# Kernel optimization log

Hardware: AMD Instinct MI355X
Metric: run time of the kernel (lower is better)

Reference implementation:

```python
import jax, jax.numpy as jnp
import numpy as np

N = 50000   # n_nodes
E = 800000  # n_edges (directed)
D = 64      # feature dim (in = hidden = out = 64 per source)


def setup_inputs() -> dict:
    key = jax.random.key(0)
    ks = jax.random.split(key, 16)
    s = 0.1  # init scale
    inp = {
        "x": jax.random.normal(ks[0], (N, D), jnp.float32),
        "edge_index": jax.random.randint(ks[1], (2, E), 0, N),
        # GCNConv 1
        "W1": jax.random.normal(ks[2], (D, 64), jnp.float32) * s,
        "b1": jnp.zeros((64,), jnp.float32),
        # TransformerConv (heads=1): query/key/value + root (skip) linear
        "Wq": jax.random.normal(ks[3], (64, 64), jnp.float32) * s,
        "bq": jnp.zeros((64,), jnp.float32),
        "Wk": jax.random.normal(ks[4], (64, 64), jnp.float32) * s,
        "bk": jnp.zeros((64,), jnp.float32),
        "Wv": jax.random.normal(ks[5], (64, 64), jnp.float32) * s,
        "bv": jnp.zeros((64,), jnp.float32),
        "Ws": jax.random.normal(ks[6], (64, 64), jnp.float32) * s,
        "bs": jnp.zeros((64,), jnp.float32),
        # GCNConv 2
        "W2": jax.random.normal(ks[7], (64, D), jnp.float32) * s,
        "b2": jnp.zeros((D,), jnp.float32),
    }
    return inp


def gcn_conv(x, W, b, src, dst, n):
    """PyG GCNConv: symmetric normalization with self-loops, then scatter-add."""
    xw = x @ W  # [N, F]
    loop = jnp.arange(n)
    src2 = jnp.concatenate([src, loop])
    dst2 = jnp.concatenate([dst, loop])
    deg = jax.ops.segment_sum(jnp.ones(src2.shape[0], xw.dtype), dst2, num_segments=n)
    dinv = jnp.where(deg > 0, jax.lax.rsqrt(deg), 0.0)
    norm = dinv[src2] * dinv[dst2]  # [E+N]
    out = jax.ops.segment_sum(xw[src2] * norm[:, None], dst2, num_segments=n)
    return out + b


def segment_softmax(logits, seg, n):
    m = jax.ops.segment_max(logits, seg, num_segments=n)
    e = jnp.exp(logits - m[seg])
    z = jax.ops.segment_sum(e, seg, num_segments=n)
    return e / z[seg]


def transformer_conv(x, Wq, bq, Wk, bk, Wv, bv, Ws, bs, src, dst, n):
    """PyG TransformerConv (heads=1, concat=True, root_weight=True)."""
    q = x @ Wq + bq  # [N, 64]
    k = x @ Wk + bk
    v = x @ Wv + bv
    scale = jax.lax.rsqrt(jnp.asarray(q.shape[-1], q.dtype))
    logits = jnp.sum(q[dst] * k[src], axis=-1) * scale  # [E]
    alpha = segment_softmax(logits, dst, n)
    aggr = jax.ops.segment_sum(v[src] * alpha[:, None], dst, num_segments=n)
    return aggr + x @ Ws + bs  # root/skip connection


def reference(x, edge_index, W1, b1, Wq, bq, Wk, bk, Wv, bv, Ws, bs, W2, b2):
    src, dst = edge_index[0], edge_index[1]
    n = x.shape[0]
    x1 = jax.nn.relu(gcn_conv(x, W1, b1, src, dst, n))
    x2 = transformer_conv(x1, Wq, bq, Wk, bk, Wv, bv, Ws, bs, src, dst, n)
    x3 = gcn_conv(x2, W2, b2, src, dst, n)
    return x3
```

## Files before the change

### kernel.cpp

```cpp
#include <hip/hip_runtime.h>
#include <math.h>


#define D 64
#define BKT_SHIFT 9
#define CAP 12288
#define CHUNK 4096

__device__ __forceinline__ unsigned short f2bf(float f) {
    unsigned int u = __float_as_uint(f);
    u += 0x7FFFu + ((u >> 16) & 1u);
    return (unsigned short)(u >> 16);
}
#define BF_LO(u) __uint_as_float((u) << 16)
#define BF_HI(u) __uint_as_float((u) & 0xFFFF0000u)


__global__ void init_gcursor(int* __restrict__ gcursor) {
    if (threadIdx.x < 128) gcursor[threadIdx.x] = 0;
}

__global__ __launch_bounds__(256) void binA_kernel(const int* __restrict__ src,
                                                   const int* __restrict__ dst,
                                                   int* __restrict__ gcursor,
                                                   unsigned int* __restrict__ staging,
                                                   int e, int nbkt) {
    __shared__ int cntB[128];
    __shared__ int offB[128];
    __shared__ int curB[128];
    __shared__ int gbase[128];
    __shared__ unsigned int pairs[CHUNK];
    __shared__ unsigned char bkt[CHUNK];

    int t = threadIdx.x;
    int e0 = blockIdx.x * CHUNK;
    int ecnt = min(CHUNK, e - e0);

    if (t < 128) cntB[t] = 0;
    __syncthreads();

    int myS[CHUNK / 256], myD[CHUNK / 256];
    #pragma unroll
    for (int i = 0; i < CHUNK / 256; ++i) {
        int idx = t + 256 * i;
        if (idx < ecnt) {
            myS[i] = src[e0 + idx];
            myD[i] = dst[e0 + idx];
            atomicAdd(&cntB[myD[i] >> BKT_SHIFT], 1);
        }
    }
    __syncthreads();
    if (t < 128) offB[t] = cntB[t];
    __syncthreads();
    for (int off = 1; off < 128; off <<= 1) {
        int add = (t < 128 && t >= off) ? offB[t - off] : 0;
        __syncthreads();
        if (t < 128) offB[t] += add;
        __syncthreads();
    }
    if (t < 128) {
        int excl = offB[t] - cntB[t];
        offB[t] = excl;
        curB[t] = excl;
        if (t < nbkt && cntB[t] > 0) gbase[t] = atomicAdd(&gcursor[t], cntB[t]);
    }
    __syncthreads();
    #pragma unroll
    for (int i = 0; i < CHUNK / 256; ++i) {
        int idx = t + 256 * i;
        if (idx < ecnt) {
            int b = myD[i] >> BKT_SHIFT;
            int p = atomicAdd(&curB[b], 1);
            pairs[p] = ((unsigned int)myD[i] << 16) | (unsigned int)myS[i];
            bkt[p] = (unsigned char)b;
        }
    }
    __syncthreads();
    for (int p = t; p < ecnt; p += 256) {
        int b = bkt[p];
        staging[(size_t)b * CAP + gbase[b] + (p - offB[b])] = pairs[p];
    }
}

__global__ __launch_bounds__(256) void binB_kernel(const int* __restrict__ gcursor,
                                                   const unsigned int* __restrict__ staging,
                                                   unsigned short* __restrict__ esrc,
                                                   int* __restrict__ cnt,
                                                   int* __restrict__ rowptr,
                                                   float* __restrict__ dinv,
                                                   int n, int nbkt) {
    __shared__ int bpre[128];
    __shared__ int c512[512];
    __shared__ int o512[512];
    int t = threadIdx.x;
    int b = blockIdx.x;

    if (t < 128) bpre[t] = (t < nbkt) ? gcursor[t] : 0;
    __syncthreads();
    for (int off = 1; off < 128; off <<= 1) {
        int add = (t < 128 && t >= off) ? bpre[t - off] : 0;
        __syncthreads();
        if (t < 128) bpre[t] += add;
        __syncthreads();
    }
    int base_b = (b == 0) ? 0 : bpre[b - 1];
    int cnt_b = gcursor[b];
    int lo = b << BKT_SHIFT;

    c512[t] = 0; c512[t + 256] = 0;
    __syncthreads();
    const unsigned int* st = staging + (size_t)b * CAP;
    for (int i = t; i < cnt_b; i += 256)
        atomicAdd(&c512[(int)(st[i] >> 16) - lo], 1);
    __syncthreads();
    o512[t] = c512[t]; o512[t + 256] = c512[t + 256];
    __syncthreads();
    for (int off = 1; off < 512; off <<= 1) {
        int a1 = (t >= off) ? o512[t - off] : 0;
        int a2 = o512[t + 256 - off];
        __syncthreads();
        o512[t] += a1; o512[t + 256] += a2;
        __syncthreads();
    }
    int e1 = o512[t] - c512[t];
    int e2 = o512[t + 256] - c512[t + 256];
    __syncthreads();
    o512[t] = e1; o512[t + 256] = e2;
    __syncthreads();
    for (int i = t; i < 512; i += 256) {
        int g = lo + i;
        if (g < n) {
            int c = c512[i];
            cnt[g] = c;
            rowptr[g] = base_b + o512[i];
            dinv[g] = rsqrtf((float)c + 1.0f);
        }
    }
    __syncthreads();
    for (int i = t; i < cnt_b; i += 256) {
        unsigned int pk = st[i];
        int local = (int)(pk >> 16) - lo;
        int p = atomicAdd(&o512[local], 1);
        esrc[base_b + p] = (unsigned short)(pk & 0xFFFFu);
    }
}

__global__ __launch_bounds__(256) void gemm64_bf16s(const float* __restrict__ X,
                                                    const float* __restrict__ W,
                                                    const float* __restrict__ dinv,
                                                    unsigned short* __restrict__ xs, int n) {
    __shared__ float sX[64][68];
    __shared__ float sW[64 * 64];
    int t = threadIdx.x;
    int base = blockIdx.x * 64;
    #pragma unroll
    for (int i = 0; i < 4; ++i) {
        int f = t * 4 + i * 1024;
        *(float4*)&sW[f] = *(const float4*)&W[f];
        int r = f >> 6, c = f & 63;
        int row = base + r;
        float4 xv = (row < n) ? *(const float4*)&X[(size_t)row * D + c]
                              : make_float4(0.f, 0.f, 0.f, 0.f);
        *(float4*)&sX[r][c] = xv;
    }
    __syncthreads();

    int cg = t & 15, rg = t >> 4;
    int j0 = cg * 4, r0 = rg * 4;
    float acc[4][4];
    #pragma unroll
    for (int a = 0; a < 4; ++a)
        #pragma unroll
        for (int c = 0; c < 4; ++c) acc[a][c] = 0.0f;

    #pragma unroll 4
    for (int kk = 0; kk < 64; kk += 4) {
        float4 w0 = *(const float4*)&sW[(kk + 0) * 64 + j0];
        float4 w1 = *(const float4*)&sW[(kk + 1) * 64 + j0];
        float4 w2 = *(const float4*)&sW[(kk + 2) * 64 + j0];
        float4 w3 = *(const float4*)&sW[(kk + 3) * 64 + j0];
        #pragma unroll
        for (int a = 0; a < 4; ++a) {
            float4 xv = *(const float4*)&sX[r0 + a][kk];
            acc[a][0] = fmaf(xv.x, w0.x, acc[a][0]); acc[a][1] = fmaf(xv.x, w0.y, acc[a][1]);
            acc[a][2] = fmaf(xv.x, w0.z, acc[a][2]); acc[a][3] = fmaf(xv.x, w0.w, acc[a][3]);
            acc[a][0] = fmaf(xv.y, w1.x, acc[a][0]); acc[a][1] = fmaf(xv.y, w1.y, acc[a][1]);
            acc[a][2] = fmaf(xv.y, w1.z, acc[a][2]); acc[a][3] = fmaf(xv.y, w1.w, acc[a][3]);
            acc[a][0] = fmaf(xv.z, w2.x, acc[a][0]); acc[a][1] = fmaf(xv.z, w2.y, acc[a][1]);
            acc[a][2] = fmaf(xv.z, w2.z, acc[a][2]); acc[a][3] = fmaf(xv.z, w2.w, acc[a][3]);
            acc[a][0] = fmaf(xv.w, w3.x, acc[a][0]); acc[a][1] = fmaf(xv.w, w3.y, acc[a][1]);
            acc[a][2] = fmaf(xv.w, w3.z, acc[a][2]); acc[a][3] = fmaf(xv.w, w3.w, acc[a][3]);
        }
    }

    #pragma unroll
    for (int a = 0; a < 4; ++a) {
        int row = base + r0 + a;
        if (row < n) {
            float dv = dinv[row];
            ushort4 h;
            h.x = f2bf(acc[a][0] * dv);
            h.y = f2bf(acc[a][1] * dv);
            h.z = f2bf(acc[a][2] * dv);
            h.w = f2bf(acc[a][3] * dv);
            *(ushort4*)&xs[(size_t)row * D + j0] = h;
        }
    }
}

__global__ __launch_bounds__(256) void fusedA_kernel(const unsigned short* __restrict__ xs,
                                                     const float* __restrict__ dinv,
                                                     const int* __restrict__ rowptr,
                                                     const int* __restrict__ cnt,
                                                     const unsigned short* __restrict__ esrc,
                                                     const float* __restrict__ b1,
                                                     const float* __restrict__ Wq,
                                                     const float* __restrict__ bq,
                                                     const float* __restrict__ Wk,
                                                     const float* __restrict__ bk,
                                                     const float* __restrict__ Wv,
                                                     const float* __restrict__ bv,
                                                     const float* __restrict__ Ws,
                                                     const float* __restrict__ bs,
                                                     float* __restrict__ Yq,
                                                     unsigned short* __restrict__ kv,
                                                     float* __restrict__ Ysk, int n) {
    __shared__ float sX[32][68];
    __shared__ float sW[64 * 64];
    int t = threadIdx.x;
    int base = blockIdx.x * 32;
    int local = t >> 3, sub = t & 7;
    int j0 = sub * 8;
    int node = base + local;

    {
        float a[8] = {0.f, 0.f, 0.f, 0.f, 0.f, 0.f, 0.f, 0.f};
        float4 o0 = make_float4(0.f, 0.f, 0.f, 0.f);
        float4 o1 = make_float4(0.f, 0.f, 0.f, 0.f);
        if (node < n) {
            float dd = dinv[node];
            int start = rowptr[node], deg = cnt[node];
            uint4 sr = *(const uint4*)&xs[(size_t)node * D + j0];
            a[0] += BF_LO(sr.x); a[1] += BF_HI(sr.x);
            a[2] += BF_LO(sr.y); a[3] += BF_HI(sr.y);
            a[4] += BF_LO(sr.z); a[5] += BF_HI(sr.z);
            a[6] += BF_LO(sr.w); a[7] += BF_HI(sr.w);
            int i = 0;
            for (; i + 8 <= deg; i += 8) {
                uint4 r[8];
                #pragma unroll
                for (int u = 0; u < 8; ++u) {
                    int s = esrc[start + i + u];
                    r[u] = *(const uint4*)&xs[(size_t)s * D + j0];
                }
                #pragma unroll
                for (int u = 0; u < 8; ++u) {
                    a[0] += BF_LO(r[u].x); a[1] += BF_HI(r[u].x);
                    a[2] += BF_LO(r[u].y); a[3] += BF_HI(r[u].y);
                    a[4] += BF_LO(r[u].z); a[5] += BF_HI(r[u].z);
                    a[6] += BF_LO(r[u].w); a[7] += BF_HI(r[u].w);
                }
            }
            for (; i + 4 <= deg; i += 4) {
                uint4 r[4];
                #pragma unroll
                for (int u = 0; u < 4; ++u) {
                    int s = esrc[start + i + u];
                    r[u] = *(const uint4*)&xs[(size_t)s * D + j0];
                }
                #pragma unroll
                for (int u = 0; u < 4; ++u) {
                    a[0] += BF_LO(r[u].x); a[1] += BF_HI(r[u].x);
                    a[2] += BF_LO(r[u].y); a[3] += BF_HI(r[u].y);
                    a[4] += BF_LO(r[u].z); a[5] += BF_HI(r[u].z);
                    a[6] += BF_LO(r[u].w); a[7] += BF_HI(r[u].w);
                }
            }
            for (; i < deg; ++i) {
                int s = esrc[start + i];
                uint4 r = *(const uint4*)&xs[(size_t)s * D + j0];
                a[0] += BF_LO(r.x); a[1] += BF_HI(r.x);
                a[2] += BF_LO(r.y); a[3] += BF_HI(r.y);
                a[4] += BF_LO(r.z); a[5] += BF_HI(r.z);
                a[6] += BF_LO(r.w); a[7] += BF_HI(r.w);
            }
            float4 bb0 = *(const float4*)&b1[j0];
            float4 bb1 = *(const float4*)&b1[j0 + 4];
            o0.x = fmaxf(fmaf(dd, a[0], bb0.x), 0.f);
            o0.y = fmaxf(fmaf(dd, a[1], bb0.y), 0.f);
            o0.z = fmaxf(fmaf(dd, a[2], bb0.z), 0.f);
            o0.w = fmaxf(fmaf(dd, a[3], bb0.w), 0.f);
            o1.x = fmaxf(fmaf(dd, a[4], bb1.x), 0.f);
            o1.y = fmaxf(fmaf(dd, a[5], bb1.y), 0.f);
            o1.z = fmaxf(fmaf(dd, a[6], bb1.z), 0.f);
            o1.w = fmaxf(fmaf(dd, a[7], bb1.w), 0.f);
        }
        *(float4*)&sX[local][j0] = o0;
        *(float4*)&sX[local][j0 + 4] = o1;
    }

    int cg = t & 15, rg = t >> 4;
    int gj0 = cg * 4, r0 = rg * 2;

    #pragma unroll 1
    for (int w4 = 0; w4 < 4; ++w4) {
        const float* W = (w4 == 0) ? Wq : (w4 == 1) ? Wk : (w4 == 2) ? Wv : Ws;
        const float* B = (w4 == 0) ? bq : (w4 == 1) ? bk : (w4 == 2) ? bv : bs;
        __syncthreads();
        #pragma unroll
        for (int i = 0; i < 4; ++i) {
            int f = t * 4 + i * 1024;
            *(float4*)&sW[f] = *(const float4*)&W[f];
        }
        __syncthreads();

        float acc[2][4];
        #pragma unroll
        for (int a = 0; a < 2; ++a)
            #pragma unroll
            for (int c = 0; c < 4; ++c) acc[a][c] = 0.0f;

        #pragma unroll 4
        for (int kk = 0; kk < 64; kk += 4) {
            float4 w0 = *(const float4*)&sW[(kk + 0) * 64 + gj0];
            float4 w1 = *(const float4*)&sW[(kk + 1) * 64 + gj0];
            float4 w2 = *(const float4*)&sW[(kk + 2) * 64 + gj0];
            float4 w3 = *(const float4*)&sW[(kk + 3) * 64 + gj0];
            #pragma unroll
            for (int a = 0; a < 2; ++a) {
                float4 xv = *(const float4*)&sX[r0 + a][kk];
                acc[a][0] = fmaf(xv.x, w0.x, acc[a][0]); acc[a][1] = fmaf(xv.x, w0.y, acc[a][1]);
                acc[a][2] = fmaf(xv.x, w0.z, acc[a][2]); acc[a][3] = fmaf(xv.x, w0.w, acc[a][3]);
                acc[a][0] = fmaf(xv.y, w1.x, acc[a][0]); acc[a][1] = fmaf(xv.y, w1.y, acc[a][1]);
                acc[a][2] = fmaf(xv.y, w1.z, acc[a][2]); acc[a][3] = fmaf(xv.y, w1.w, acc[a][3]);
                acc[a][0] = fmaf(xv.z, w2.x, acc[a][0]); acc[a][1] = fmaf(xv.z, w2.y, acc[a][1]);
                acc[a][2] = fmaf(xv.z, w2.z, acc[a][2]); acc[a][3] = fmaf(xv.z, w2.w, acc[a][3]);
                acc[a][0] = fmaf(xv.w, w3.x, acc[a][0]); acc[a][1] = fmaf(xv.w, w3.y, acc[a][1]);
                acc[a][2] = fmaf(xv.w, w3.z, acc[a][2]); acc[a][3] = fmaf(xv.w, w3.w, acc[a][3]);
            }
        }

        float4 bb = *(const float4*)&B[gj0];
        if (w4 == 0) {
            #pragma unroll
            for (int a = 0; a < 2; ++a) {
                int row = base + r0 + a;
                if (row < n) {
                    float4 o = make_float4((acc[a][0] + bb.x) * 0.125f,
                                           (acc[a][1] + bb.y) * 0.125f,
                                           (acc[a][2] + bb.z) * 0.125f,
                                           (acc[a][3] + bb.w) * 0.125f);
                    *(float4*)&Yq[(size_t)row * D + gj0] = o;
                }
            }
        } else if (w4 == 3) {
            #pragma unroll
            for (int a = 0; a < 2; ++a) {
                int row = base + r0 + a;
                if (row < n) {
                    float4 o = make_float4(acc[a][0] + bb.x, acc[a][1] + bb.y,
                                           acc[a][2] + bb.z, acc[a][3] + bb.w);
                    *(float4*)&Ysk[(size_t)row * D + gj0] = o;
                }
            }
        } else {
            int off = (w4 == 1) ? 0 : 64;
            #pragma unroll
            for (int a = 0; a < 2; ++a) {
                int row = base + r0 + a;
                if (row < n) {
                    ushort4 h;
                    h.x = f2bf(acc[a][0] + bb.x);
                    h.y = f2bf(acc[a][1] + bb.y);
                    h.z = f2bf(acc[a][2] + bb.z);
                    h.w = f2bf(acc[a][3] + bb.w);
                    *(ushort4*)&kv[(size_t)row * 128 + off + gj0] = h;
                }
            }
        }
    }
}

__global__ __launch_bounds__(256) void fusedB_kernel(const float* __restrict__ q,
                                                     const unsigned short* __restrict__ kv,
                                                     const float* __restrict__ skip,
                                                     const float* __restrict__ dinv,
                                                     const int* __restrict__ rowptr,
                                                     const int* __restrict__ cnt,
                                                     const unsigned short* __restrict__ esrc,
                                                     const float* __restrict__ W2,
                                                     unsigned short* __restrict__ xs2, int n) {
    __shared__ float sX[32][68];
    __shared__ float sW[64 * 64];
    int t = threadIdx.x;
    int base = blockIdx.x * 32;
    int local = t >> 3, sub = t & 7;
    int j0 = sub * 8;
    int node = base + local;

    #pragma unroll
    for (int i = 0; i < 4; ++i) {
        int f = t * 4 + i * 1024;
        *(float4*)&sW[f] = *(const float4*)&W2[f];
    }

    {
        float4 o0 = make_float4(0.f, 0.f, 0.f, 0.f);
        float4 o1 = make_float4(0.f, 0.f, 0.f, 0.f);
        if (node < n) {
            int start = rowptr[node], deg = cnt[node];
            float4 q0 = *(const float4*)&q[(size_t)node * D + j0];
            float4 q1 = *(const float4*)&q[(size_t)node * D + j0 + 4];
            float4 s0 = *(const float4*)&skip[(size_t)node * D + j0];
            float4 s1 = *(const float4*)&skip[(size_t)node * D + j0 + 4];
            float z = 0.0f;
            float a[8] = {0.f, 0.f, 0.f, 0.f, 0.f, 0.f, 0.f, 0.f};
            int i = 0;
            for (; i + 8 <= deg; i += 8) {
                size_t ro[8];
                #pragma unroll
                for (int u = 0; u < 8; ++u)
                    ro[u] = (size_t)esrc[start + i + u] * 128;
                float w[8];
                {
                    uint4 kr[8];
                    #pragma unroll
                    for (int u = 0; u < 8; ++u)
                        kr[u] = *(const uint4*)&kv[ro[u] + j0];
                    float p[8];
                    #pragma unroll
                    for (int u = 0; u < 8; ++u)
                        p[u] = q0.x * BF_LO(kr[u].x) + q0.y * BF_HI(kr[u].x)
                             + q0.z * BF_LO(kr[u].y) + q0.w * BF_HI(kr[u].y)
                             + q1.x * BF_LO(kr[u].z) + q1.y * BF_HI(kr[u].z)
                             + q1.z * BF_LO(kr[u].w) + q1.w * BF_HI(kr[u].w);
                    #pragma unroll
                    for (int off = 1; off < 8; off <<= 1) {
                        #pragma unroll
                        for (int u = 0; u < 8; ++u) p[u] += __shfl_xor(p[u], off, 64);
                    }
                    #pragma unroll
                    for (int u = 0; u < 8; ++u) {
                        w[u] = __expf(p[u]);
                        z += w[u];
                    }
                }
                {
                    uint4 vr[8];
                    #pragma unroll
                    for (int u = 0; u < 8; ++u)
                        vr[u] = *(const uint4*)&kv[ro[u] + 64 + j0];
                    #pragma unroll
                    for (int u = 0; u < 8; ++u) {
                        a[0] = fmaf(w[u], BF_LO(vr[u].x), a[0]);
                        a[1] = fmaf(w[u], BF_HI(vr[u].x), a[1]);
                        a[2] = fmaf(w[u], BF_LO(vr[u].y), a[2]);
                        a[3] = fmaf(w[u], BF_HI(vr[u].y), a[3]);
                        a[4] = fmaf(w[u], BF_LO(vr[u].z), a[4]);
                        a[5] = fmaf(w[u], BF_HI(vr[u].z), a[5]);
                        a[6] = fmaf(w[u], BF_LO(vr[u].w), a[6]);
                        a[7] = fmaf(w[u], BF_HI(vr[u].w), a[7]);
                    }
                }
            }
            for (; i < deg; ++i) {
                size_t ro = (size_t)esrc[start + i] * 128;
                uint4 kr = *(const uint4*)&kv[ro + j0];
                uint4 vr = *(const uint4*)&kv[ro + 64 + j0];
                float p = q0.x * BF_LO(kr.x) + q0.y * BF_HI(kr.x)
                        + q0.z * BF_LO(kr.y) + q0.w * BF_HI(kr.y)
                        + q1.x * BF_LO(kr.z) + q1.y * BF_HI(kr.z)
                        + q1.z * BF_LO(kr.w) + q1.w * BF_HI(kr.w);
                #pragma unroll
                for (int off = 1; off < 8; off <<= 1) p += __shfl_xor(p, off, 64);
                float w = __expf(p);
                z += w;
                a[0] = fmaf(w, BF_LO(vr.x), a[0]); a[1] = fmaf(w, BF_HI(vr.x), a[1]);
                a[2] = fmaf(w, BF_LO(vr.y), a[2]); a[3] = fmaf(w, BF_HI(vr.y), a[3]);
                a[4] = fmaf(w, BF_LO(vr.z), a[4]); a[5] = fmaf(w, BF_HI(vr.z), a[5]);
                a[6] = fmaf(w, BF_LO(vr.w), a[6]); a[7] = fmaf(w, BF_HI(vr.w), a[7]);
            }
            if (deg > 0) {
                float inv = 1.0f / z;
                o0.x = fmaf(a[0], inv, s0.x); o0.y = fmaf(a[1], inv, s0.y);
                o0.z = fmaf(a[2], inv, s0.z); o0.w = fmaf(a[3], inv, s0.w);
                o1.x = fmaf(a[4], inv, s1.x); o1.y = fmaf(a[5], inv, s1.y);
                o1.z = fmaf(a[6], inv, s1.z); o1.w = fmaf(a[7], inv, s1.w);
            } else {
                o0 = s0; o1 = s1;
            }
        }
        *(float4*)&sX[local][j0] = o0;
        *(float4*)&sX[local][j0 + 4] = o1;
    }
    __syncthreads();

    int cg = t & 15, rg = t >> 4;
    int gj0 = cg * 4, r0 = rg * 2;
    float acc[2][4];
    #pragma unroll
    for (int a = 0; a < 2; ++a)
        #pragma unroll
        for (int c = 0; c < 4; ++c) acc[a][c] = 0.0f;

    #pragma unroll 4
    for (int kk = 0; kk < 64; kk += 4) {
        float4 w0 = *(const float4*)&sW[(kk + 0) * 64 + gj0];
        float4 w1 = *(const float4*)&sW[(kk + 1) * 64 + gj0];
        float4 w2 = *(const float4*)&sW[(kk + 2) * 64 + gj0];
        float4 w3 = *(const float4*)&sW[(kk + 3) * 64 + gj0];
        #pragma unroll
        for (int a = 0; a < 2; ++a) {
            float4 xv = *(const float4*)&sX[r0 + a][kk];
            acc[a][0] = fmaf(xv.x, w0.x, acc[a][0]); acc[a][1] = fmaf(xv.x, w0.y, acc[a][1]);
            acc[a][2] = fmaf(xv.x, w0.z, acc[a][2]); acc[a][3] = fmaf(xv.x, w0.w, acc[a][3]);
            acc[a][0] = fmaf(xv.y, w1.x, acc[a][0]); acc[a][1] = fmaf(xv.y, w1.y, acc[a][1]);
            acc[a][2] = fmaf(xv.y, w1.z, acc[a][2]); acc[a][3] = fmaf(xv.y, w1.w, acc[a][3]);
            acc[a][0] = fmaf(xv.z, w2.x, acc[a][0]); acc[a][1] = fmaf(xv.z, w2.y, acc[a][1]);
            acc[a][2] = fmaf(xv.z, w2.z, acc[a][2]); acc[a][3] = fmaf(xv.z, w2.w, acc[a][3]);
            acc[a][0] = fmaf(xv.w, w3.x, acc[a][0]); acc[a][1] = fmaf(xv.w, w3.y, acc[a][1]);
            acc[a][2] = fmaf(xv.w, w3.z, acc[a][2]); acc[a][3] = fmaf(xv.w, w3.w, acc[a][3]);
        }
    }

    #pragma unroll
    for (int a = 0; a < 2; ++a) {
        int row = base + r0 + a;
        if (row < n) {
            float dv = dinv[row];
            ushort4 h;
            h.x = f2bf(acc[a][0] * dv);
            h.y = f2bf(acc[a][1] * dv);
            h.z = f2bf(acc[a][2] * dv);
            h.w = f2bf(acc[a][3] * dv);
            *(ushort4*)&xs2[(size_t)row * D + gj0] = h;
        }
    }
}

__global__ __launch_bounds__(256) void gcn_gather_kernel(const unsigned short* __restrict__ xs,
                                                         const float* __restrict__ dinv,
                                                         const int* __restrict__ rowptr,
                                                         const int* __restrict__ cnt,
                                                         const unsigned short* __restrict__ esrc,
                                                         const float* __restrict__ bias,
                                                         float* __restrict__ out,
                                                         int n, int relu) {
    int node = (blockIdx.x * blockDim.x + threadIdx.x) >> 6;
    if (node >= n) return;
    int lane = threadIdx.x & 63;
    int grp = lane >> 3;
    int sub = lane & 7;
    int j0 = sub * 8;

    int start = rowptr[node], deg = cnt[node];

    float a[8] = {0.f, 0.f, 0.f, 0.f, 0.f, 0.f, 0.f, 0.f};
    int i = grp;
    int sNext = (i < deg) ? esrc[start + i] : 0;
    for (; i < deg; i += 8) {
        int s = sNext;
        int in = i + 8;
        if (in < deg) sNext = esrc[start + in];
        uint4 r = *(const uint4*)&xs[(size_t)s * D + j0];
        a[0] += BF_LO(r.x); a[1] += BF_HI(r.x);
        a[2] += BF_LO(r.y); a[3] += BF_HI(r.y);
        a[4] += BF_LO(r.z); a[5] += BF_HI(r.z);
        a[6] += BF_LO(r.w); a[7] += BF_HI(r.w);
    }
    #pragma unroll
    for (int off = 8; off < 64; off <<= 1) {
        #pragma unroll
        for (int c = 0; c < 8; ++c) a[c] += __shfl_xor(a[c], off, 64);
    }

    if (grp == 0) {
        float dd = dinv[node];
        uint4 sr = *(const uint4*)&xs[(size_t)node * D + j0];
        a[0] += BF_LO(sr.x); a[1] += BF_HI(sr.x);
        a[2] += BF_LO(sr.y); a[3] += BF_HI(sr.y);
        a[4] += BF_LO(sr.z); a[5] += BF_HI(sr.z);
        a[6] += BF_LO(sr.w); a[7] += BF_HI(sr.w);
        float4 b0 = *(const float4*)&bias[j0];
        float4 b1 = *(const float4*)&bias[j0 + 4];
        float o[8];
        o[0] = fmaf(dd, a[0], b0.x); o[1] = fmaf(dd, a[1], b0.y);
        o[2] = fmaf(dd, a[2], b0.z); o[3] = fmaf(dd, a[3], b0.w);
        o[4] = fmaf(dd, a[4], b1.x); o[5] = fmaf(dd, a[5], b1.y);
        o[6] = fmaf(dd, a[6], b1.z); o[7] = fmaf(dd, a[7], b1.w);
        if (relu) {
            #pragma unroll
            for (int c = 0; c < 8; ++c) o[c] = fmaxf(o[c], 0.f);
        }
        *(float4*)&out[(size_t)node * D + j0] = make_float4(o[0], o[1], o[2], o[3]);
        *(float4*)&out[(size_t)node * D + j0 + 4] = make_float4(o[4], o[5], o[6], o[7]);
    }
}


extern "C" void kernel_launch(void* const* d_in, const int* in_sizes, int n_in,
                              void* d_out, int out_size, void* d_ws, size_t ws_size,
                              hipStream_t stream) {
    const float* x  = (const float*)d_in[0];
    const int*   ei = (const int*)d_in[1];
    const float* W1 = (const float*)d_in[2];
    const float* b1 = (const float*)d_in[3];
    const float* Wq = (const float*)d_in[4];
    const float* bq = (const float*)d_in[5];
    const float* Wk = (const float*)d_in[6];
    const float* bk = (const float*)d_in[7];
    const float* Wv = (const float*)d_in[8];
    const float* bv = (const float*)d_in[9];
    const float* Ws = (const float*)d_in[10];
    const float* bs = (const float*)d_in[11];
    const float* W2 = (const float*)d_in[12];
    const float* b2 = (const float*)d_in[13];
    float* out = (float*)d_out;

    const int n = in_sizes[0] / D;
    const int e = in_sizes[1] / 2;
    const int* src = ei;
    const int* dst = ei + e;
    const int n64 = n * D;
    const int nbkt = (n + (1 << BKT_SHIFT) - 1) >> BKT_SHIFT;

    char* w = (char*)d_ws;
    auto carve = [&](size_t bytes) {
        char* p = w;
        w += (bytes + 255) & ~(size_t)255;
        return p;
    };
    int* gcursor            = (int*)carve(128 * 4);
    unsigned int* staging   = (unsigned int*)carve((size_t)nbkt * CAP * 4);
    unsigned short* esrc    = (unsigned short*)carve((size_t)e * 2);
    int* cnt                = (int*)carve((size_t)n * 4);
    int* rowptr             = (int*)carve((size_t)n * 4);
    float* dinv             = (float*)carve((size_t)n * 4);
    float* bufQ             = (float*)carve((size_t)n64 * 4);
    unsigned short* xs      = (unsigned short*)carve((size_t)n64 * 2);
    unsigned short* kv      = (unsigned short*)carve((size_t)n64 * 4);

    const int nb_binA = (e + CHUNK - 1) / CHUNK;
    const int nb_nw   = (n + 3) / 4;
    const int nb_g    = (n + 63) / 64;
    const int nb_f    = (n + 31) / 32;

    init_gcursor<<<1, 128, 0, stream>>>(gcursor);
    binA_kernel<<<nb_binA, 256, 0, stream>>>(src, dst, gcursor, staging, e, nbkt);
    binB_kernel<<<nbkt, 256, 0, stream>>>(gcursor, staging, esrc, cnt, rowptr, dinv, n, nbkt);

    gemm64_bf16s<<<nb_g, 256, 0, stream>>>(x, W1, dinv, xs, n);

    fusedA_kernel<<<nb_f, 256, 0, stream>>>(xs, dinv, rowptr, cnt, esrc, b1,
                                            Wq, bq, Wk, bk, Wv, bv, Ws, bs,
                                            bufQ, kv, out, n);

    fusedB_kernel<<<nb_f, 256, 0, stream>>>(bufQ, kv, out, dinv,
                                            rowptr, cnt, esrc, W2, xs, n);

    gcn_gather_kernel<<<nb_nw, 256, 0, stream>>>(xs, dinv, rowptr, cnt, esrc,
                                                 b2, out, n, 0);
}
```

Measured before the change: 241.7 us.

## Restructure fused kernels' dense projections with bf16 transposed weights and larger tiles

```diff
diff --git a/kernel.cpp b/kernel.cpp
--- a/kernel.cpp
+++ b/kernel.cpp
@@ -208,7 +208,7 @@
     }
 }
 
-__global__ __launch_bounds__(256) void fusedA_kernel(const unsigned short* __restrict__ xs,
+__global__ __launch_bounds__(512) void fusedA_kernel(const unsigned short* __restrict__ xs,
                                                      const float* __restrict__ dinv,
                                                      const int* __restrict__ rowptr,
                                                      const int* __restrict__ cnt,
@@ -225,13 +225,31 @@
                                                      float* __restrict__ Yq,
                                                      unsigned short* __restrict__ kv,
                                                      float* __restrict__ Ysk, int n) {
-    __shared__ float sX[32][68];
-    __shared__ float sW[64 * 64];
+    __shared__ float sX[64][68];
+    __shared__ unsigned short sWt[256 * 72];
     int t = threadIdx.x;
-    int base = blockIdx.x * 32;
+    int base = blockIdx.x * 64;
     int local = t >> 3, sub = t & 7;
     int j0 = sub * 8;
     int node = base + local;
+
+    {
+        int k0 = t >> 4;
+        int c0 = (t & 15) * 4;
+        #pragma unroll
+        for (int m = 0; m < 4; ++m) {
+            const float* W = (m == 0) ? Wq : (m == 1) ? Wk : (m == 2) ? Wv : Ws;
+            #pragma unroll
+            for (int h = 0; h < 2; ++h) {
+                int k = k0 + 32 * h;
+                float4 w = *(const float4*)&W[k * 64 + c0];
+                sWt[(m * 64 + c0 + 0) * 72 + k] = f2bf(w.x);
+                sWt[(m * 64 + c0 + 1) * 72 + k] = f2bf(w.y);
+                sWt[(m * 64 + c0 + 2) * 72 + k] = f2bf(w.z);
+                sWt[(m * 64 + c0 + 3) * 72 + k] = f2bf(w.w);
+            }
+        }
+    }
 
     {
         float a[8] = {0.f, 0.f, 0.f, 0.f, 0.f, 0.f, 0.f, 0.f};
@@ -261,21 +279,6 @@
                     a[6] += BF_LO(r[u].w); a[7] += BF_HI(r[u].w);
                 }
             }
-            for (; i + 4 <= deg; i += 4) {
-                uint4 r[4];
-                #pragma unroll
-                for (int u = 0; u < 4; ++u) {
-                    int s = esrc[start + i + u];
-                    r[u] = *(const uint4*)&xs[(size_t)s * D + j0];
-                }
-                #pragma unroll
-                for (int u = 0; u < 4; ++u) {
-                    a[0] += BF_LO(r[u].x); a[1] += BF_HI(r[u].x);
-                    a[2] += BF_LO(r[u].y); a[3] += BF_HI(r[u].y);
-                    a[4] += BF_LO(r[u].z); a[5] += BF_HI(r[u].z);
-                    a[6] += BF_LO(r[u].w); a[7] += BF_HI(r[u].w);
-                }
-            }
             for (; i < deg; ++i) {
                 int s = esrc[start + i];
                 uint4 r = *(const uint4*)&xs[(size_t)s * D + j0];
@@ -298,90 +301,69 @@
         *(float4*)&sX[local][j0] = o0;
         *(float4*)&sX[local][j0 + 4] = o1;
     }
-
-    int cg = t & 15, rg = t >> 4;
-    int gj0 = cg * 4, r0 = rg * 2;
-
-    #pragma unroll 1
-    for (int w4 = 0; w4 < 4; ++w4) {
-        const float* W = (w4 == 0) ? Wq : (w4 == 1) ? Wk : (w4 == 2) ? Wv : Ws;
-        const float* B = (w4 == 0) ? bq : (w4 == 1) ? bk : (w4 == 2) ? bv : bs;
-        __syncthreads();
-        #pragma unroll
-        for (int i = 0; i < 4; ++i) {
-            int f = t * 4 + i * 1024;
-            *(float4*)&sW[f] = *(const float4*)&W[f];
-        }
-        __syncthreads();
-
-        float acc[2][4];
-        #pragma unroll
-        for (int a = 0; a < 2; ++a)
+    __syncthreads();
+
+    int rg = t >> 5;
+    int cg = t & 31;
+    float acc[4][8];
+    #pragma unroll
+    for (int a = 0; a < 4; ++a)
+        #pragma unroll
+        for (int j = 0; j < 8; ++j) acc[a][j] = 0.0f;
+
+    #pragma unroll 2
+    for (int s = 0; s < 8; ++s) {
+        float xv[4][8];
+        #pragma unroll
+        for (int a = 0; a < 4; ++a) {
+            int row = rg + 16 * a;
+            float4 x0 = *(const float4*)&sX[row][s * 8];
+            float4 x1 = *(const float4*)&sX[row][s * 8 + 4];
+            xv[a][0] = x0.x; xv[a][1] = x0.y; xv[a][2] = x0.z; xv[a][3] = x0.w;
+            xv[a][4] = x1.x; xv[a][5] = x1.y; xv[a][6] = x1.z; xv[a][7] = x1.w;
+        }
+        #pragma unroll
+        for (int j = 0; j < 8; ++j) {
+            uint4 wc = *(const uint4*)&sWt[(cg + 32 * j) * 72 + s * 8];
+            float w0 = BF_LO(wc.x), w1 = BF_HI(wc.x);
+            float w2 = BF_LO(wc.y), w3 = BF_HI(wc.y);
+            float w4 = BF_LO(wc.z), w5 = BF_HI(wc.z);
+            float w6 = BF_LO(wc.w), w7 = BF_HI(wc.w);
             #pragma unroll
-            for (int c = 0; c < 4; ++c) acc[a][c] = 0.0f;
-
-        #pragma unroll 4
-        for (int kk = 0; kk < 64; kk += 4) {
-            float4 w0 = *(const float4*)&sW[(kk + 0) * 64 + gj0];
-            float4 w1 = *(const float4*)&sW[(kk + 1) * 64 + gj0];
-            float4 w2 = *(const float4*)&sW[(kk + 2) * 64 + gj0];
-            float4 w3 = *(const float4*)&sW[(kk + 3) * 64 + gj0];
-            #pragma unroll
-            for (int a = 0; a < 2; ++a) {
-                float4 xv = *(const float4*)&sX[r0 + a][kk];
-                acc[a][0] = fmaf(xv.x, w0.x, acc[a][0]); acc[a][1] = fmaf(xv.x, w0.y, acc[a][1]);
-                acc[a][2] = fmaf(xv.x, w0.z, acc[a][2]); acc[a][3] = fmaf(xv.x, w0.w, acc[a][3]);
-                acc[a][0] = fmaf(xv.y, w1.x, acc[a][0]); acc[a][1] = fmaf(xv.y, w1.y, acc[a][1]);
-                acc[a][2] = fmaf(xv.y, w1.z, acc[a][2]); acc[a][3] = fmaf(xv.y, w1.w, acc[a][3]);
-                acc[a][0] = fmaf(xv.z, w2.x, acc[a][0]); acc[a][1] = fmaf(xv.z, w2.y, acc[a][1]);
-                acc[a][2] = fmaf(xv.z, w2.z, acc[a][2]); acc[a][3] = fmaf(xv.z, w2.w, acc[a][3]);
-                acc[a][0] = fmaf(xv.w, w3.x, acc[a][0]); acc[a][1] = fmaf(xv.w, w3.y, acc[a][1]);
-                acc[a][2] = fmaf(xv.w, w3.z, acc[a][2]); acc[a][3] = fmaf(xv.w, w3.w, acc[a][3]);
-            }
-        }
-
-        float4 bb = *(const float4*)&B[gj0];
-        if (w4 == 0) {
-            #pragma unroll
-            for (int a = 0; a < 2; ++a) {
-                int row = base + r0 + a;
-                if (row < n) {
-                    float4 o = make_float4((acc[a][0] + bb.x) * 0.125f,
-                                           (acc[a][1] + bb.y) * 0.125f,
-                                           (acc[a][2] + bb.z) * 0.125f,
-                                           (acc[a][3] + bb.w) * 0.125f);
-                    *(float4*)&Yq[(size_t)row * D + gj0] = o;
-                }
-            }
-        } else if (w4 == 3) {
-            #pragma unroll
-            for (int a = 0; a < 2; ++a) {
-                int row = base + r0 + a;
-                if (row < n) {
-                    float4 o = make_float4(acc[a][0] + bb.x, acc[a][1] + bb.y,
-                                           acc[a][2] + bb.z, acc[a][3] + bb.w);
-                    *(float4*)&Ysk[(size_t)row * D + gj0] = o;
-                }
-            }
-        } else {
-            int off = (w4 == 1) ? 0 : 64;
-            #pragma unroll
-            for (int a = 0; a < 2; ++a) {
-                int row = base + r0 + a;
-                if (row < n) {
-                    ushort4 h;
-                    h.x = f2bf(acc[a][0] + bb.x);
-                    h.y = f2bf(acc[a][1] + bb.y);
-                    h.z = f2bf(acc[a][2] + bb.z);
-                    h.w = f2bf(acc[a][3] + bb.w);
-                    *(ushort4*)&kv[(size_t)row * 128 + off + gj0] = h;
-                }
-            }
-        }
-    }
-}
-
-__global__ __launch_bounds__(256) void fusedB_kernel(const float* __restrict__ q,
+            for (int a = 0; a < 4; ++a) {
+                acc[a][j] = fmaf(xv[a][0], w0, acc[a][j]);
+                acc[a][j] = fmaf(xv[a][1], w1, acc[a][j]);
+                acc[a][j] = fmaf(xv[a][2], w2, acc[a][j]);
+                acc[a][j] = fmaf(xv[a][3], w3, acc[a][j]);
+                acc[a][j] = fmaf(xv[a][4], w4, acc[a][j]);
+                acc[a][j] = fmaf(xv[a][5], w5, acc[a][j]);
+                acc[a][j] = fmaf(xv[a][6], w6, acc[a][j]);
+                acc[a][j] = fmaf(xv[a][7], w7, acc[a][j]);
+            }
+        }
+    }
+
+    float bq0 = bq[cg], bq1 = bq[cg + 32];
+    float bk0 = bk[cg], bk1 = bk[cg + 32];
+    float bv0 = bv[cg], bv1 = bv[cg + 32];
+    float bs0 = bs[cg], bs1 = bs[cg + 32];
+    #pragma unroll
+    for (int a = 0; a < 4; ++a) {
+        int row = base + rg + 16 * a;
+        if (row < n) {
+            Yq[(size_t)row * 64 + cg]        = (acc[a][0] + bq0) * 0.125f;
+            Yq[(size_t)row * 64 + cg + 32]   = (acc[a][1] + bq1) * 0.125f;
+            kv[(size_t)row * 128 + cg]       = f2bf(acc[a][2] + bk0);
+            kv[(size_t)row * 128 + cg + 32]  = f2bf(acc[a][3] + bk1);
+            kv[(size_t)row * 128 + 64 + cg]      = f2bf(acc[a][4] + bv0);
+            kv[(size_t)row * 128 + 64 + cg + 32] = f2bf(acc[a][5] + bv1);
+            Ysk[(size_t)row * 64 + cg]       = acc[a][6] + bs0;
+            Ysk[(size_t)row * 64 + cg + 32]  = acc[a][7] + bs1;
+        }
+    }
+}
+
+__global__ __launch_bounds__(512) void fusedB_kernel(const float* __restrict__ q,
                                                      const unsigned short* __restrict__ kv,
                                                      const float* __restrict__ skip,
                                                      const float* __restrict__ dinv,
@@ -390,18 +372,26 @@
                                                      const unsigned short* __restrict__ esrc,
                                                      const float* __restrict__ W2,
                                                      unsigned short* __restrict__ xs2, int n) {
-    __shared__ float sX[32][68];
-    __shared__ float sW[64 * 64];
+    __shared__ float sX[64][68];
+    __shared__ unsigned short sWt[64 * 72];
     int t = threadIdx.x;
-    int base = blockIdx.x * 32;
+    int base = blockIdx.x * 64;
     int local = t >> 3, sub = t & 7;
     int j0 = sub * 8;
     int node = base + local;
 
-    #pragma unroll
-    for (int i = 0; i < 4; ++i) {
-        int f = t * 4 + i * 1024;
-        *(float4*)&sW[f] = *(const float4*)&W2[f];
+    {
+        int k0 = t >> 4;
+        int c0 = (t & 15) * 4;
+        #pragma unroll
+        for (int h = 0; h < 2; ++h) {
+            int k = k0 + 32 * h;
+            float4 w = *(const float4*)&W2[k * 64 + c0];
+            sWt[(c0 + 0) * 72 + k] = f2bf(w.x);
+            sWt[(c0 + 1) * 72 + k] = f2bf(w.y);
+            sWt[(c0 + 2) * 72 + k] = f2bf(w.z);
+            sWt[(c0 + 3) * 72 + k] = f2bf(w.w);
+        }
     }
 
     {
@@ -495,45 +485,54 @@
     }
     __syncthreads();
 
-    int cg = t & 15, rg = t >> 4;
-    int gj0 = cg * 4, r0 = rg * 2;
+    int rg = t >> 4;
+    int cg = t & 15;
     float acc[2][4];
     #pragma unroll
     for (int a = 0; a < 2; ++a)
         #pragma unroll
-        for (int c = 0; c < 4; ++c) acc[a][c] = 0.0f;
-
-    #pragma unroll 4
-    for (int kk = 0; kk < 64; kk += 4) {
-        float4 w0 = *(const float4*)&sW[(kk + 0) * 64 + gj0];
-        float4 w1 = *(const float4*)&sW[(kk + 1) * 64 + gj0];
-        float4 w2 = *(const float4*)&sW[(kk + 2) * 64 + gj0];
-        float4 w3 = *(const float4*)&sW[(kk + 3) * 64 + gj0];
+        for (int j = 0; j < 4; ++j) acc[a][j] = 0.0f;
+
+    #pragma unroll 2
+    for (int s = 0; s < 8; ++s) {
+        float xv[2][8];
         #pragma unroll
         for (int a = 0; a < 2; ++a) {
-            float4 xv = *(const float4*)&sX[r0 + a][kk];
-            acc[a][0] = fmaf(xv.x, w0.x, acc[a][0]); acc[a][1] = fmaf(xv.x, w0.y, acc[a][1]);
-            acc[a][2] = fmaf(xv.x, w0.z, acc[a][2]); acc[a][3] = fmaf(xv.x, w0.w, acc[a][3]);
-            acc[a][0] = fmaf(xv.y, w1.x, acc[a][0]); acc[a][1] = fmaf(xv.y, w1.y, acc[a][1]);
-            acc[a][2] = fmaf(xv.y, w1.z, acc[a][2]); acc[a][3] = fmaf(xv.y, w1.w, acc[a][3]);
-            acc[a][0] = fmaf(xv.z, w2.x, acc[a][0]); acc[a][1] = fmaf(xv.z, w2.y, acc[a][1]);
-            acc[a][2] = fmaf(xv.z, w2.z, acc[a][2]); acc[a][3] = fmaf(xv.z, w2.w, acc[a][3]);
-            acc[a][0] = fmaf(xv.w, w3.x, acc[a][0]); acc[a][1] = fmaf(xv.w, w3.y, acc[a][1]);
-            acc[a][2] = fmaf(xv.w, w3.z, acc[a][2]); acc[a][3] = fmaf(xv.w, w3.w, acc[a][3]);
+            int row = rg + 32 * a;
+            float4 x0 = *(const float4*)&sX[row][s * 8];
+            float4 x1 = *(const float4*)&sX[row][s * 8 + 4];
+            xv[a][0] = x0.x; xv[a][1] = x0.y; xv[a][2] = x0.z; xv[a][3] = x0.w;
+            xv[a][4] = x1.x; xv[a][5] = x1.y; xv[a][6] = x1.z; xv[a][7] = x1.w;
+        }
+        #pragma unroll
+        for (int j = 0; j < 4; ++j) {
+            uint4 wc = *(const uint4*)&sWt[(cg + 16 * j) * 72 + s * 8];
+            float w0 = BF_LO(wc.x), w1 = BF_HI(wc.x);
+            float w2 = BF_LO(wc.y), w3 = BF_HI(wc.y);
+            float w4 = BF_LO(wc.z), w5 = BF_HI(wc.z);
+            float w6 = BF_LO(wc.w), w7 = BF_HI(wc.w);
+            #pragma unroll
+            for (int a = 0; a < 2; ++a) {
+                acc[a][j] = fmaf(xv[a][0], w0, acc[a][j]);
+                acc[a][j] = fmaf(xv[a][1], w1, acc[a][j]);
+                acc[a][j] = fmaf(xv[a][2], w2, acc[a][j]);
+                acc[a][j] = fmaf(xv[a][3], w3, acc[a][j]);
+                acc[a][j] = fmaf(xv[a][4], w4, acc[a][j]);
+                acc[a][j] = fmaf(xv[a][5], w5, acc[a][j]);
+                acc[a][j] = fmaf(xv[a][6], w6, acc[a][j]);
+                acc[a][j] = fmaf(xv[a][7], w7, acc[a][j]);
+            }
         }
     }
 
     #pragma unroll
     for (int a = 0; a < 2; ++a) {
-        int row = base + r0 + a;
+        int row = base + rg + 32 * a;
         if (row < n) {
             float dv = dinv[row];
-            ushort4 h;
-            h.x = f2bf(acc[a][0] * dv);
-            h.y = f2bf(acc[a][1] * dv);
-            h.z = f2bf(acc[a][2] * dv);
-            h.w = f2bf(acc[a][3] * dv);
-            *(ushort4*)&xs2[(size_t)row * D + gj0] = h;
+            #pragma unroll
+            for (int j = 0; j < 4; ++j)
+                xs2[(size_t)row * 64 + cg + 16 * j] = f2bf(acc[a][j] * dv);
         }
     }
 }
@@ -643,7 +642,6 @@
     const int nb_binA = (e + CHUNK - 1) / CHUNK;
     const int nb_nw   = (n + 3) / 4;
     const int nb_g    = (n + 63) / 64;
-    const int nb_f    = (n + 31) / 32;
 
     init_gcursor<<<1, 128, 0, stream>>>(gcursor);
     binA_kernel<<<nb_binA, 256, 0, stream>>>(src, dst, gcursor, staging, e, nbkt);
@@ -651,11 +649,11 @@
 
     gemm64_bf16s<<<nb_g, 256, 0, stream>>>(x, W1, dinv, xs, n);
 
-    fusedA_kernel<<<nb_f, 256, 0, stream>>>(xs, dinv, rowptr, cnt, esrc, b1,
+    fusedA_kernel<<<nb_g, 512, 0, stream>>>(xs, dinv, rowptr, cnt, esrc, b1,
                                             Wq, bq, Wk, bk, Wv, bv, Ws, bs,
                                             bufQ, kv, out, n);
 
-    fusedB_kernel<<<nb_f, 256, 0, stream>>>(bufQ, kv, out, dinv,
+    fusedB_kernel<<<nb_g, 512, 0, stream>>>(bufQ, kv, out, dinv,
                                             rowptr, cnt, esrc, W2, xs, n);
 
     gcn_gather_kernel<<<nb_nw, 256, 0, stream>>>(xs, dinv, rowptr, cnt, esrc,
```

Result: slower. 251.4 us (+4.0%).
